# Kernel optimization log

Measured on AMD Instinct MI355X. Metric: run time of the kernel, lower is better.

The kernel has to match this reference:

```python
import jax, jax.numpy as jnp
import numpy as np

EMBED = 1024
HEAD = 128
B, T = 4, 4096


def setup_inputs() -> dict:
    key = jax.random.key(0)
    k1, k2, k3, k4 = jax.random.split(key, 4)
    context = jax.random.normal(k1, (B, T, EMBED), dtype=jnp.float32)
    # nn.Linear(embedding_size, head_size, bias=False): y = x @ W^T; store W^T as [C, H]
    s = 1.0 / np.sqrt(EMBED)
    Wk = jax.random.normal(k2, (EMBED, HEAD), dtype=jnp.float32) * s
    Wq = jax.random.normal(k3, (EMBED, HEAD), dtype=jnp.float32) * s
    Wv = jax.random.normal(k4, (EMBED, HEAD), dtype=jnp.float32) * s
    return {"context": context, "Wk": Wk, "Wq": Wq, "Wv": Wv}


def reference(context, Wk, Wq, Wv):
    Bc, Tc, C = context.shape
    k = jnp.einsum("btc,ch->bth", context, Wk)
    q = jnp.einsum("btc,ch->bth", context, Wq)
    v = jnp.einsum("btc,ch->bth", context, Wv)
    # NOTE: original scales by 1/sqrt(C) (embedding size), not 1/sqrt(head_size)
    scale = 1.0 / jnp.sqrt(jnp.float32(C))
    scores = jnp.einsum("bqh,bkh->bqk", q, k) * scale  # [B, T, T]
    causal = jnp.tril(jnp.ones((Tc, Tc), dtype=bool))
    scores = jnp.where(causal, scores, -jnp.inf)
    attn = jax.nn.softmax(scores, axis=-1)
    # dropout_rate = 0.0 (eval-mode): no-op
    out = jnp.einsum("bqk,bkh->bqh", attn, v)
    return out
```

## Files before the change

kernel.cpp:

```cpp
#include <hip/hip_runtime.h>
#include <cstdint>
#include <cstddef>

#define EMBED 1024
#define HEAD  128
#define BATCH 4
#define SEQ   4096
#define KSC   0.04508422f

typedef __attribute__((ext_vector_type(4))) float f32x4;
typedef __attribute__((ext_vector_type(16))) float f32x16;
typedef __attribute__((ext_vector_type(8))) short s16x8;
typedef __attribute__((ext_vector_type(4))) int i32x4;
typedef __attribute__((ext_vector_type(4))) unsigned short u16x4;

__device__ __forceinline__ unsigned short f2bf(float f) {
    union { float f; unsigned u; } v; v.f = f;
    unsigned r = v.u + 0x7fffu + ((v.u >> 16) & 1u);
    return (unsigned short)(r >> 16);
}

__device__ __forceinline__ int cvtpk(float lo, float hi_) {
    int r;
    asm("v_cvt_pk_bf16_f32 %0, %1, %2" : "=v"(r) : "v"(lo), "v"(hi_));
    return r;
}

__global__ __launch_bounds__(256) void wt_kernel(const float* __restrict__ Wq,
                                                 const float* __restrict__ Wk,
                                                 const float* __restrict__ Wv,
                                                 unsigned short* __restrict__ Wt) {
    __shared__ __align__(16) float Lw[32 * 132];
    const int tid = threadIdx.x;
    const int sel = blockIdx.x >> 5;
    const int k0  = (blockIdx.x & 31) * 32;
    const float* W = (sel == 0) ? Wq : (sel == 1) ? Wk : Wv;
    #pragma unroll
    for (int t = 0; t < 4; ++t) {
        int c = tid + t * 256;
        int kk = c >> 5, hc = c & 31;
        *(f32x4*)&Lw[kk * 132 + hc * 4] =
            *(const f32x4*)(W + (size_t)(k0 + kk) * HEAD + hc * 4);
    }
    __syncthreads();
    #pragma unroll
    for (int t = 0; t < 2; ++t) {
        int c = tid + t * 256;
        int h = c >> 2, cg = c & 3;
        int p0 = cvtpk(Lw[(cg * 8 + 0) * 132 + h], Lw[(cg * 8 + 1) * 132 + h]);
        int p1 = cvtpk(Lw[(cg * 8 + 2) * 132 + h], Lw[(cg * 8 + 3) * 132 + h]);
        int p2 = cvtpk(Lw[(cg * 8 + 4) * 132 + h], Lw[(cg * 8 + 5) * 132 + h]);
        int p3 = cvtpk(Lw[(cg * 8 + 6) * 132 + h], Lw[(cg * 8 + 7) * 132 + h]);
        i32x4 pk = {p0, p1, p2, p3};
        *(s16x8*)(Wt + (size_t)(sel * 128 + h) * EMBED + k0 + cg * 8) = *(s16x8*)&pk;
    }
}

__global__ __launch_bounds__(256) void proj_kernel(const float* __restrict__ ctx,
                                                   const unsigned short* __restrict__ Wt,
                                                   unsigned short* __restrict__ Qb,
                                                   unsigned short* __restrict__ Kb,
                                                   unsigned short* __restrict__ Vtb) {
    __shared__ __align__(16) short As[64 * 72];
    __shared__ __align__(16) short Bs[128 * 72];
    const int tid = threadIdx.x;
    const int lane = tid & 63, w = tid >> 6;
    const int wr = w >> 1, wc = w & 1;
    const int lr = lane & 15, lk = lane >> 4;
    const int m0 = blockIdx.x * 64;
    const int sel = blockIdx.y;
    const unsigned short* Wts = Wt + (size_t)sel * 131072;

    f32x4 zero = {0.f, 0.f, 0.f, 0.f};
    f32x4 acc[2][4];
    #pragma unroll
    for (int i = 0; i < 2; ++i)
        #pragma unroll
        for (int jn = 0; jn < 4; ++jn) acc[i][jn] = zero;

    for (int kk = 0; kk < EMBED; kk += 64) {
        __syncthreads();
        #pragma unroll
        for (int t = 0; t < 2; ++t) {
            int c = tid + t * 256;
            int row = c >> 3, cg = c & 7;
            const float* src = ctx + (size_t)(m0 + row) * EMBED + kk + cg * 8;
            f32x4 x0 = *(const f32x4*)src;
            f32x4 x1 = *(const f32x4*)(src + 4);
            int p0 = cvtpk(x0[0], x0[1]);
            int p1 = cvtpk(x0[2], x0[3]);
            int p2 = cvtpk(x1[0], x1[1]);
            int p3 = cvtpk(x1[2], x1[3]);
            i32x4 pk = {p0, p1, p2, p3};
            *(s16x8*)&As[row * 72 + cg * 8] = *(s16x8*)&pk;
        }
        #pragma unroll
        for (int t = 0; t < 4; ++t) {
            int c = tid + t * 256;
            int row = c >> 3, cg = c & 7;
            *(s16x8*)&Bs[row * 72 + cg * 8] =
                *(const s16x8*)(Wts + (size_t)row * EMBED + kk + cg * 8);
        }
        __syncthreads();
        s16x8 af[2][2], bfr[4][2];
        #pragma unroll
        for (int mi = 0; mi < 2; ++mi)
            #pragma unroll
            for (int k2 = 0; k2 < 2; ++k2)
                af[mi][k2] = *(const s16x8*)&As[(wr * 32 + mi * 16 + lr) * 72 + k2 * 32 + lk * 8];
        #pragma unroll
        for (int ni = 0; ni < 4; ++ni)
            #pragma unroll
            for (int k2 = 0; k2 < 2; ++k2)
                bfr[ni][k2] = *(const s16x8*)&Bs[(wc * 64 + ni * 16 + lr) * 72 + k2 * 32 + lk * 8];
        #pragma unroll
        for (int k2 = 0; k2 < 2; ++k2)
            #pragma unroll
            for (int mi = 0; mi < 2; ++mi)
                #pragma unroll
                for (int ni = 0; ni < 4; ++ni)
                    acc[mi][ni] = __builtin_amdgcn_mfma_f32_16x16x32_bf16(af[mi][k2], bfr[ni][k2], acc[mi][ni], 0, 0, 0);
    }

    if (sel == 2) {
        #pragma unroll
        for (int mi = 0; mi < 2; ++mi) {
            int t0r = m0 + wr * 32 + mi * 16 + lk * 4;
            int b = t0r >> 12, tl = t0r & (SEQ - 1);
            #pragma unroll
            for (int ni = 0; ni < 4; ++ni) {
                int col = wc * 64 + ni * 16 + lr;
                u16x4 vv;
                #pragma unroll
                for (int r = 0; r < 4; ++r) vv[r] = f2bf(acc[mi][ni][r]);
                *(u16x4*)(Vtb + ((size_t)(b * HEAD + col)) * SEQ + tl) = vv;
            }
        }
    } else {
        unsigned short* outp = sel ? Kb : Qb;
        const float sc = sel ? 1.0f : KSC;
        #pragma unroll
        for (int mi = 0; mi < 2; ++mi) {
            int row = m0 + wr * 32 + mi * 16 + lk * 4;
            #pragma unroll
            for (int ni = 0; ni < 4; ++ni) {
                int col = wc * 64 + ni * 16 + lr;
                #pragma unroll
                for (int r = 0; r < 4; ++r)
                    outp[(size_t)(row + r) * HEAD + col] = f2bf(acc[mi][ni][r] * sc);
            }
        }
    }
}

__global__ __launch_bounds__(256, 2) void attn_kernel(const unsigned short* __restrict__ Q,
                                                      const unsigned short* __restrict__ K,
                                                      const unsigned short* __restrict__ Vt,
                                                      unsigned short* __restrict__ po,
                                                      float* __restrict__ pml) {
    __shared__ __align__(16) char smem[32768];
    const int tid = threadIdx.x;
    const int lane = tid & 63, w = tid >> 6;
    const int l31 = lane & 31, hi = lane >> 5;
    const int hi16 = hi << 4;

    const int b = blockIdx.x / 272;
    int t = blockIdx.x % 272;
    int qt = 0, cum = 0;
    while (cum + ((qt >> 1) + 1) <= t) { cum += (qt >> 1) + 1; ++qt; }
    const int c = t - cum;
    const int nj = min(4, 2 * qt + 2 - 4 * c);
    const int kb0 = c * 256;
    const int slot = b * 272 + cum + c;

    const unsigned short* qp = Q + ((size_t)(b * SEQ + qt * 128 + w * 32 + l31)) * HEAD + hi * 8;
    s16x8 qf[8];
    #pragma unroll
    for (int dt = 0; dt < 8; ++dt) qf[dt] = *(const s16x8*)(qp + dt * 16);

    f32x16 o0, o1, o2, o3;
    #pragma unroll
    for (int r = 0; r < 16; ++r) { o0[r] = 0.f; o1[r] = 0.f; o2[r] = 0.f; o3[r] = 0.f; }
    float m_run = -1e30f, l_run = 0.f;

    const int krow = tid >> 4, kch = tid & 15;
    const int vdr  = tid >> 3, vch = tid & 7;

    s16x8 kst[4], vst[4];
    #pragma unroll
    for (int p = 0; p < 4; ++p) {
        kst[p] = *(const s16x8*)(K + ((size_t)(b * SEQ + kb0 + krow + p * 16)) * HEAD + kch * 8);
        vst[p] = *(const s16x8*)(Vt + ((size_t)(b * HEAD + vdr + p * 32)) * SEQ + kb0 + vch * 8);
    }
    #pragma unroll
    for (int p = 0; p < 4; ++p) {
        int r0 = krow + p * 16;
        *(s16x8*)(smem + r0 * 256 + ((kch * 16) ^ ((r0 & 7) << 4))) = kst[p];
        int d0 = vdr + p * 32;
        *(s16x8*)(smem + 16384 + d0 * 128 + ((vch * 16) ^ ((d0 & 7) << 4))) = vst[p];
    }
    __syncthreads();

    for (int j = 0; j < nj; ++j) {
        const int kb = kb0 + j * 64;
        if (j + 1 < nj) {
            int kbn = kb + 64;
            #pragma unroll
            for (int p = 0; p < 4; ++p) {
                kst[p] = *(const s16x8*)(K + ((size_t)(b * SEQ + kbn + krow + p * 16)) * HEAD + kch * 8);
                vst[p] = *(const s16x8*)(Vt + ((size_t)(b * HEAD + vdr + p * 32)) * SEQ + kbn + vch * 8);
            }
        }

        f32x16 st0, st1;
        #pragma unroll
        for (int r = 0; r < 16; ++r) { st0[r] = 0.f; st1[r] = 0.f; }
        const int sw = (l31 & 7) << 4;
        const char* kbase0 = smem + l31 * 256;
        const char* kbase1 = kbase0 + 32 * 256;
        __builtin_amdgcn_s_setprio(1);
        #pragma unroll
        for (int dt = 0; dt < 8; ++dt) {
            s16x8 ka0 = *(const s16x8*)(kbase0 + ((dt * 32 + hi16) ^ sw));
            s16x8 ka1 = *(const s16x8*)(kbase1 + ((dt * 32 + hi16) ^ sw));
            st0 = __builtin_amdgcn_mfma_f32_32x32x16_bf16(ka0, qf[dt], st0, 0, 0, 0);
            st1 = __builtin_amdgcn_mfma_f32_32x32x16_bf16(ka1, qf[dt], st1, 0, 0, 0);
        }
        __builtin_amdgcn_s_setprio(0);

        if (4 * c + j >= 2 * qt) {
            const int qg = qt * 128 + w * 32 + l31;
            #pragma unroll
            for (int r = 0; r < 16; ++r) {
                int crow = (r & 3) + 8 * (r >> 2) + 4 * hi;
                if (kb + crow > qg)      st0[r] = -3e37f;
                if (kb + 32 + crow > qg) st1[r] = -3e37f;
            }
        }

        float mx = st0[0];
        #pragma unroll
        for (int r = 1; r < 16; ++r) mx = fmaxf(mx, st0[r]);
        #pragma unroll
        for (int r = 0; r < 16; ++r) mx = fmaxf(mx, st1[r]);
        mx = fmaxf(mx, __shfl_xor(mx, 32));
        if (!__all(mx <= m_run + 8.0f)) {
            float mn = fmaxf(m_run, mx);
            float f = exp2f(m_run - mn);
            l_run *= f;
            int fi = __float_as_int(f);
            #pragma unroll
            for (int r = 0; r < 16; ++r) {
                int srcb = 4 * ((r & 3) + 8 * (r >> 2)) + 16 * hi;
                float fr = __int_as_float(__builtin_amdgcn_ds_bpermute(srcb, fi));
                o0[r] *= fr; o1[r] *= fr; o2[r] *= fr; o3[r] *= fr;
            }
            m_run = mn;
        }
        float rs = 0.f;
        #pragma unroll
        for (int r = 0; r < 16; ++r) {
            st0[r] = exp2f(st0[r] - m_run); rs += st0[r];
            st1[r] = exp2f(st1[r] - m_run); rs += st1[r];
        }
        rs += __shfl_xor(rs, 32);
        l_run += rs;

        int a0 = cvtpk(st0[0], st0[1]),   b0 = cvtpk(st0[4], st0[5]);
        int a1 = cvtpk(st0[2], st0[3]),   b1 = cvtpk(st0[6], st0[7]);
        int a2 = cvtpk(st0[8], st0[9]),   b2 = cvtpk(st0[12], st0[13]);
        int a3 = cvtpk(st0[10], st0[11]), b3 = cvtpk(st0[14], st0[15]);
        int a4 = cvtpk(st1[0], st1[1]),   b4 = cvtpk(st1[4], st1[5]);
        int a5 = cvtpk(st1[2], st1[3]),   b5 = cvtpk(st1[6], st1[7]);
        int a6 = cvtpk(st1[8], st1[9]),   b6 = cvtpk(st1[12], st1[13]);
        int a7 = cvtpk(st1[10], st1[11]), b7 = cvtpk(st1[14], st1[15]);
        asm volatile("v_permlane32_swap_b32 %0, %1" : "+v"(a0), "+v"(b0));
        asm volatile("v_permlane32_swap_b32 %0, %1" : "+v"(a1), "+v"(b1));
        asm volatile("v_permlane32_swap_b32 %0, %1" : "+v"(a2), "+v"(b2));
        asm volatile("v_permlane32_swap_b32 %0, %1" : "+v"(a3), "+v"(b3));
        asm volatile("v_permlane32_swap_b32 %0, %1" : "+v"(a4), "+v"(b4));
        asm volatile("v_permlane32_swap_b32 %0, %1" : "+v"(a5), "+v"(b5));
        asm volatile("v_permlane32_swap_b32 %0, %1" : "+v"(a6), "+v"(b6));
        asm volatile("v_permlane32_swap_b32 %0, %1" : "+v"(a7), "+v"(b7));
        i32x4 pw0 = {a0, a1, b0, b1}; s16x8 pa0 = *(s16x8*)&pw0;
        i32x4 pw1 = {a2, a3, b2, b3}; s16x8 pa1 = *(s16x8*)&pw1;
        i32x4 pw2 = {a4, a5, b4, b5}; s16x8 pa2 = *(s16x8*)&pw2;
        i32x4 pw3 = {a6, a7, b6, b7}; s16x8 pa3 = *(s16x8*)&pw3;

        __builtin_amdgcn_s_setprio(1);
        #define PV_NT(oo, nt) { \
            const int vr = (nt) * 32 + l31; \
            const int vsw = (vr & 7) << 4; \
            const char* vb = smem + 16384 + vr * 128; \
            oo = __builtin_amdgcn_mfma_f32_32x32x16_bf16(pa0, *(const s16x8*)(vb + ((0  + hi16) ^ vsw)), oo, 0, 0, 0); \
            oo = __builtin_amdgcn_mfma_f32_32x32x16_bf16(pa1, *(const s16x8*)(vb + ((32 + hi16) ^ vsw)), oo, 0, 0, 0); \
            oo = __builtin_amdgcn_mfma_f32_32x32x16_bf16(pa2, *(const s16x8*)(vb + ((64 + hi16) ^ vsw)), oo, 0, 0, 0); \
            oo = __builtin_amdgcn_mfma_f32_32x32x16_bf16(pa3, *(const s16x8*)(vb + ((96 + hi16) ^ vsw)), oo, 0, 0, 0); }
        PV_NT(o0, 0) PV_NT(o1, 1) PV_NT(o2, 2) PV_NT(o3, 3)
        #undef PV_NT
        __builtin_amdgcn_s_setprio(0);

        if (j + 1 < nj) {
            __syncthreads();
            #pragma unroll
            for (int p = 0; p < 4; ++p) {
                int r0 = krow + p * 16;
                *(s16x8*)(smem + r0 * 256 + ((kch * 16) ^ ((r0 & 7) << 4))) = kst[p];
                int d0 = vdr + p * 32;
                *(s16x8*)(smem + 16384 + d0 * 128 + ((vch * 16) ^ ((d0 & 7) << 4))) = vst[p];
            }
            __syncthreads();
        }
    }

    unsigned short* pob = po + (size_t)slot * 16384;
    #define STORE_NT(oo, nt) { \
        _Pragma("unroll") \
        for (int r = 0; r < 16; ++r) { \
            int qin = w * 32 + (r & 3) + 8 * (r >> 2) + 4 * hi; \
            pob[qin * 128 + (nt) * 32 + l31] = f2bf(oo[r]); \
        } }
    STORE_NT(o0, 0) STORE_NT(o1, 1) STORE_NT(o2, 2) STORE_NT(o3, 3)
    #undef STORE_NT
    if (lane < 32) {
        float* pm = pml + (size_t)slot * 256 + (w * 32 + lane) * 2;
        pm[0] = m_run; pm[1] = l_run;
    }
}

__global__ __launch_bounds__(256) void combine_kernel(const unsigned short* __restrict__ po,
                                                      const float* __restrict__ pml,
                                                      float* __restrict__ out) {
    const int tid = threadIdx.x;
    const int row = blockIdx.x * 8 + (tid >> 5);
    const int l32 = tid & 31;
    const int b = row >> 12, q = row & 4095;
    const int qt = q >> 7, qr = q & 127;
    const int nc = (q >> 8) + 1;
    const int cum = ((qt >> 1) + (qt & 1)) * ((qt >> 1) + 1);
    const size_t bslot = (size_t)b * 272 + cum;

    float M = -1e30f;
    for (int cc = 0; cc < nc; ++cc)
        M = fmaxf(M, pml[(bslot + cc) * 256 + qr * 2]);
    float L = 0.f;
    f32x4 acc = {0.f, 0.f, 0.f, 0.f};
    for (int cc = 0; cc < nc; ++cc) {
        const float* pm = pml + (bslot + cc) * 256 + qr * 2;
        float wgt = exp2f(pm[0] - M);
        L += wgt * pm[1];
        u16x4 x = *(const u16x4*)(po + (bslot + cc) * 16384 + qr * 128 + l32 * 4);
        #pragma unroll
        for (int e = 0; e < 4; ++e) {
            union { unsigned u; float f; } cv; cv.u = ((unsigned)x[e]) << 16;
            acc[e] += wgt * cv.f;
        }
    }
    float inv = 1.f / L;
    f32x4 y = {acc[0] * inv, acc[1] * inv, acc[2] * inv, acc[3] * inv};
    *(f32x4*)(out + (size_t)row * HEAD + l32 * 4) = y;
}

extern "C" void kernel_launch(void* const* d_in, const int* in_sizes, int n_in,
                              void* d_out, int out_size, void* d_ws, size_t ws_size,
                              hipStream_t stream) {
    const float* ctx = (const float*)d_in[0];
    const float* Wk  = (const float*)d_in[1];
    const float* Wq  = (const float*)d_in[2];
    const float* Wv  = (const float*)d_in[3];
    float* out = (float*)d_out;

    unsigned short* Wt  = (unsigned short*)d_ws;
    unsigned short* Qb  = Wt + 3 * 131072;
    unsigned short* Kb  = Qb + 2097152;
    unsigned short* Vtb = Kb + 2097152;
    unsigned short* po  = Vtb + 2097152;
    float* pml = (float*)(po + (size_t)1088 * 16384);

    wt_kernel<<<96, 256, 0, stream>>>(Wq, Wk, Wv, Wt);
    proj_kernel<<<dim3(256, 3), 256, 0, stream>>>(ctx, Wt, Qb, Kb, Vtb);
    attn_kernel<<<1088, 256, 0, stream>>>(Qb, Kb, Vtb, po, pml);
    combine_kernel<<<2048, 256, 0, stream>>>(po, pml, out);
}
```

Baseline: 163.5 us.

## Pre-swizzle weight tiles for direct global-to-LDS loads and stage attention output stores

The weight-transpose kernel now writes bf16 weights in per-64-K-block tiles with an XOR swizzle, so the projection kernel can copy each B tile straight into LDS with global_load_lds instead of going through registers, and reads it back with the matching swizzle. Separately, the attention kernel's per-element scattered bf16 partial-output stores are first gathered in shared memory and then written out as contiguous 16-byte vector stores. Both changes aim to cut memory instruction count and improve coalescing. The cost is an extra barrier and LDS round trip in the attention epilogue, and a tighter coupling between the weight layout and the projection kernel.

Measured after the change: 165.5 us. No clear change (+1.2%).

```diff
diff --git a/kernel.cpp b/kernel.cpp
--- a/kernel.cpp
+++ b/kernel.cpp
@@ -26,33 +26,41 @@
     return r;
 }
 
+__device__ __forceinline__ void gload16(const void* g, void* l) {
+    __builtin_amdgcn_global_load_lds(
+        (const __attribute__((address_space(1))) unsigned int*)g,
+        (__attribute__((address_space(3))) unsigned int*)l, 16, 0, 0);
+}
+
 __global__ __launch_bounds__(256) void wt_kernel(const float* __restrict__ Wq,
                                                  const float* __restrict__ Wk,
                                                  const float* __restrict__ Wv,
                                                  unsigned short* __restrict__ Wt) {
-    __shared__ __align__(16) float Lw[32 * 132];
+    __shared__ __align__(16) float Lw[64 * 132];
     const int tid = threadIdx.x;
-    const int sel = blockIdx.x >> 5;
-    const int k0  = (blockIdx.x & 31) * 32;
+    const int sel = blockIdx.x >> 4;
+    const int kb  = blockIdx.x & 15;
+    const int k0  = kb * 64;
     const float* W = (sel == 0) ? Wq : (sel == 1) ? Wk : Wv;
     #pragma unroll
-    for (int t = 0; t < 4; ++t) {
-        int c = tid + t * 256;
+    for (int it = 0; it < 8; ++it) {
+        int c = tid + it * 256;
         int kk = c >> 5, hc = c & 31;
         *(f32x4*)&Lw[kk * 132 + hc * 4] =
             *(const f32x4*)(W + (size_t)(k0 + kk) * HEAD + hc * 4);
     }
     __syncthreads();
     #pragma unroll
-    for (int t = 0; t < 2; ++t) {
-        int c = tid + t * 256;
-        int h = c >> 2, cg = c & 3;
-        int p0 = cvtpk(Lw[(cg * 8 + 0) * 132 + h], Lw[(cg * 8 + 1) * 132 + h]);
-        int p1 = cvtpk(Lw[(cg * 8 + 2) * 132 + h], Lw[(cg * 8 + 3) * 132 + h]);
-        int p2 = cvtpk(Lw[(cg * 8 + 4) * 132 + h], Lw[(cg * 8 + 5) * 132 + h]);
-        int p3 = cvtpk(Lw[(cg * 8 + 6) * 132 + h], Lw[(cg * 8 + 7) * 132 + h]);
+    for (int it = 0; it < 4; ++it) {
+        int c = tid + it * 256;
+        int h = c >> 3, sl = c & 7;
+        int phys = sl ^ (h & 7);
+        int p0 = cvtpk(Lw[(sl * 8 + 0) * 132 + h], Lw[(sl * 8 + 1) * 132 + h]);
+        int p1 = cvtpk(Lw[(sl * 8 + 2) * 132 + h], Lw[(sl * 8 + 3) * 132 + h]);
+        int p2 = cvtpk(Lw[(sl * 8 + 4) * 132 + h], Lw[(sl * 8 + 5) * 132 + h]);
+        int p3 = cvtpk(Lw[(sl * 8 + 6) * 132 + h], Lw[(sl * 8 + 7) * 132 + h]);
         i32x4 pk = {p0, p1, p2, p3};
-        *(s16x8*)(Wt + (size_t)(sel * 128 + h) * EMBED + k0 + cg * 8) = *(s16x8*)&pk;
+        *(s16x8*)(Wt + (size_t)sel * 131072 + kb * 8192 + h * 64 + phys * 8) = *(s16x8*)&pk;
     }
 }
 
@@ -62,7 +70,7 @@
                                                    unsigned short* __restrict__ Kb,
                                                    unsigned short* __restrict__ Vtb) {
     __shared__ __align__(16) short As[64 * 72];
-    __shared__ __align__(16) short Bs[128 * 72];
+    __shared__ __align__(16) short Bs[128 * 64];
     const int tid = threadIdx.x;
     const int lane = tid & 63, w = tid >> 6;
     const int wr = w >> 1, wc = w & 1;
@@ -78,8 +86,15 @@
         #pragma unroll
         for (int jn = 0; jn < 4; ++jn) acc[i][jn] = zero;
 
-    for (int kk = 0; kk < EMBED; kk += 64) {
+    for (int kkb = 0; kkb < 16; ++kkb) {
         __syncthreads();
+        const char* gb = (const char*)Wts + kkb * 16384;
+        #pragma unroll
+        for (int i = 0; i < 4; ++i) {
+            int chunk = w * 4 + i;
+            gload16(gb + chunk * 1024 + lane * 16, (char*)Bs + chunk * 1024);
+        }
+        const int kk = kkb * 64;
         #pragma unroll
         for (int t = 0; t < 2; ++t) {
             int c = tid + t * 256;
@@ -94,13 +109,6 @@
             i32x4 pk = {p0, p1, p2, p3};
             *(s16x8*)&As[row * 72 + cg * 8] = *(s16x8*)&pk;
         }
-        #pragma unroll
-        for (int t = 0; t < 4; ++t) {
-            int c = tid + t * 256;
-            int row = c >> 3, cg = c & 7;
-            *(s16x8*)&Bs[row * 72 + cg * 8] =
-                *(const s16x8*)(Wts + (size_t)row * EMBED + kk + cg * 8);
-        }
         __syncthreads();
         s16x8 af[2][2], bfr[4][2];
         #pragma unroll
@@ -111,8 +119,11 @@
         #pragma unroll
         for (int ni = 0; ni < 4; ++ni)
             #pragma unroll
-            for (int k2 = 0; k2 < 2; ++k2)
-                bfr[ni][k2] = *(const s16x8*)&Bs[(wc * 64 + ni * 16 + lr) * 72 + k2 * 32 + lk * 8];
+            for (int k2 = 0; k2 < 2; ++k2) {
+                int rB = wc * 64 + ni * 16 + lr;
+                int phys = (k2 * 4 + lk) ^ (rB & 7);
+                bfr[ni][k2] = *(const s16x8*)((const char*)Bs + rB * 128 + phys * 16);
+            }
         #pragma unroll
         for (int k2 = 0; k2 < 2; ++k2)
             #pragma unroll
@@ -313,15 +324,23 @@
         }
     }
 
-    unsigned short* pob = po + (size_t)slot * 16384;
+    __syncthreads();
+    short* os = (short*)smem;
     #define STORE_NT(oo, nt) { \
         _Pragma("unroll") \
         for (int r = 0; r < 16; ++r) { \
             int qin = w * 32 + (r & 3) + 8 * (r >> 2) + 4 * hi; \
-            pob[qin * 128 + (nt) * 32 + l31] = f2bf(oo[r]); \
+            os[qin * 128 + (nt) * 32 + l31] = (short)f2bf(oo[r]); \
         } }
     STORE_NT(o0, 0) STORE_NT(o1, 1) STORE_NT(o2, 2) STORE_NT(o3, 3)
     #undef STORE_NT
+    unsigned short* pob = po + (size_t)slot * 16384 + w * 4096;
+    const short* osw = os + w * 4096;
+    #pragma unroll
+    for (int jj = 0; jj < 8; ++jj) {
+        s16x8 v = *(const s16x8*)(osw + jj * 512 + lane * 8);
+        *(s16x8*)(pob + jj * 512 + lane * 8) = v;
+    }
     if (lane < 32) {
         float* pm = pml + (size_t)slot * 256 + (w * 32 + lane) * 2;
         pm[0] = m_run; pm[1] = l_run;
@@ -377,7 +396,7 @@
     unsigned short* po  = Vtb + 2097152;
     float* pml = (float*)(po + (size_t)1088 * 16384);
 
-    wt_kernel<<<96, 256, 0, stream>>>(Wq, Wk, Wv, Wt);
+    wt_kernel<<<48, 256, 0, stream>>>(Wq, Wk, Wv, Wt);
     proj_kernel<<<dim3(256, 3), 256, 0, stream>>>(ctx, Wt, Qb, Kb, Vtb);
     attn_kernel<<<1088, 256, 0, stream>>>(Qb, Kb, Vtb, po, pml);
     combine_kernel<<<2048, 256, 0, stream>>>(po, pml, out);
```
